# Kernel optimization log

Hardware: AMD Instinct MI355X
Metric: run time of the kernel (lower is better)

The kernel has to match this reference:

```python
import jax, jax.numpy as jnp
import numpy as np

K = 51           # kernel_size
DENSE_INNER = 2
EPS_LN = 1e-6
EPS_GRN = 1e-6

def _make_peripheral_coords(radius, dense_inner=2):
    coords = list(range(0, min(radius, dense_inner) + 1))
    v = 1
    while v < radius:
        v *= 2
        if v > dense_inner and v < radius:
            coords.append(v)
    if radius not in coords:
        coords.append(radius)
    return sorted(set(coords))

def _quantise(a, coords):
    q = 0
    for c in coords:
        if c <= a:
            q = c
        else:
            break
    return q

def _build_idx_map(kernel_size, dense_inner):
    radius = kernel_size // 2
    coords = _make_peripheral_coords(radius, dense_inner)
    signed = [-c for c in reversed(coords[1:])] + list(coords)
    P = len(signed)
    c2i = {c: i for i, c in enumerate(signed)}
    idx = []
    for i in range(kernel_size):
        oi = i - radius
        qi = _quantise(abs(oi), coords)
        ii = c2i[-qi if oi < 0 else qi]
        for j in range(kernel_size):
            oj = j - radius
            qj = _quantise(abs(oj), coords)
            jj = c2i[-qj if oj < 0 else qj]
            idx.append(ii * P + jj)
    return np.asarray(idx, dtype=np.int32), P

IDX_MAP, P = _build_idx_map(K, DENSE_INNER)  # P == 13 for K=51

DIM = 384
HID = 4 * DIM

def setup_inputs() -> dict:
    key = jax.random.key(0)
    ks = jax.random.split(key, 10)
    B, C, H, W = 8, DIM, 64, 64
    std = 0.02
    return {
        "x": jax.random.normal(ks[0], (B, C, H, W), jnp.float32),
        "weight_comp": jax.random.normal(ks[1], (C, P * P), jnp.float32) * std,
        "kpe": jax.random.normal(ks[2], (1, 1, K, K), jnp.float32) * std,
        "ln_w": jnp.ones((C,), jnp.float32),
        "ln_b": jnp.zeros((C,), jnp.float32),
        "w1": jax.random.normal(ks[3], (C, HID), jnp.float32) * std,
        "b1": jnp.zeros((HID,), jnp.float32),
        "grn_gamma": jax.random.normal(ks[4], (HID,), jnp.float32) * std,
        "grn_beta": jax.random.normal(ks[5], (HID,), jnp.float32) * std,
        "w2": jax.random.normal(ks[6], (HID, C), jnp.float32) * std,
        "b2": jnp.zeros((C,), jnp.float32),
    }

def _block(x, weight_comp, kpe, ln_w, ln_b, w1, b1, grn_gamma, grn_beta, w2, b2):
    C = x.shape[1]
    # gather-built peripheral depthwise kernel: (C, 1, K, K) + shared positional bias
    w = weight_comp[:, IDX_MAP].reshape(C, 1, K, K) + kpe
    y = jax.lax.conv_general_dilated(
        x, w, window_strides=(1, 1), padding=[(K // 2, K // 2)] * 2,
        feature_group_count=C, dimension_numbers=("NCHW", "OIHW", "NCHW"))
    h = y.transpose(0, 2, 3, 1)  # NHWC
    # LayerNorm (channels_last, biased variance, eps=1e-6)
    mu = jnp.mean(h, axis=-1, keepdims=True)
    var = jnp.mean(jnp.square(h - mu), axis=-1, keepdims=True)
    h = (h - mu) * jax.lax.rsqrt(var + EPS_LN) * ln_w + ln_b
    # pointwise MLP with GRN
    h = jnp.einsum("nhwc,cf->nhwf", h, w1) + b1
    h = jax.nn.gelu(h, approximate=False)  # nn.GELU default is exact erf form
    gx = jnp.sqrt(jnp.sum(jnp.square(h), axis=(1, 2), keepdims=True))  # (N,1,1,F)
    nx = gx / (jnp.mean(gx, axis=-1, keepdims=True) + EPS_GRN)
    h = grn_gamma * (h * nx) + grn_beta + h
    h = jnp.einsum("nhwf,fc->nhwc", h, w2) + b2
    return x + h.transpose(0, 3, 1, 2)

def reference(x, weight_comp, kpe, ln_w, ln_b, w1, b1, grn_gamma, grn_beta, w2, b2):
    return _block(x, weight_comp, kpe, ln_w, ln_b, w1, b1, grn_gamma, grn_beta, w2, b2)
```

## Files before the change

### kernel.cpp

```cpp
#include <hip/hip_runtime.h>

#define CDIM 384
#define FDIM 1536
#define KK 51
#define RAD 25
#define NPIX 32768
#define HW 4096

#define CSTR 136
#define OSTR 68

typedef float  f32x4  __attribute__((ext_vector_type(4)));
typedef short  short8 __attribute__((ext_vector_type(8)));
typedef __bf16 bf16x8 __attribute__((ext_vector_type(8)));
typedef unsigned short us4 __attribute__((ext_vector_type(4)));

__device__ __constant__ int AXIS[51] = {
  0,
  1,1,1,1,1,1,1,1,1,
  2,2,2,2,2,2,2,2,
  3,3,3,3,
  4,4,
  5,
  6,
  7,
  8,8,
  9,9,9,9,
  10,10,10,10,10,10,10,10,
  11,11,11,11,11,11,11,11,11,
  12
};

__device__ __forceinline__ unsigned short bf16_rn(float x){
  union { float f; unsigned u; } v; v.f = x;
  unsigned r = v.u + 0x7FFFu + ((v.u >> 16) & 1u);
  return (unsigned short)(r >> 16);
}
__device__ __forceinline__ unsigned short f2bf(float x){
  __bf16 h = (__bf16)x;
  return __builtin_bit_cast(unsigned short, h);
}
__device__ __forceinline__ float bf2f(unsigned short h){
  union { unsigned u; float f; } v; v.u = ((unsigned)h) << 16; return v.f;
}

__global__ __launch_bounds__(256) void k_prep(const float* __restrict__ wc,
                                              const float* __restrict__ kpe,
                                              float* __restrict__ wfull,
                                              const float* __restrict__ w1,
                                              unsigned short* __restrict__ w1T,
                                              const float* __restrict__ w2,
                                              unsigned short* __restrict__ w2T,
                                              const float* __restrict__ beta,
                                              const float* __restrict__ b2,
                                              float* __restrict__ c2,
                                              float* __restrict__ grn){
  __shared__ float tile[64][65];
  __shared__ float red[256];
  int bid = blockIdx.x;
  int tid = threadIdx.x;
  if (bid < 384){
    int c = bid;
    const float* wcc = wc + c*169;
    float* wo = wfull + (size_t)c*2601;
    for (int idx = tid; idx < 2601; idx += 256){
      int i = idx / 51, j = idx - i*51;
      wo[idx] = wcc[AXIS[i]*13 + AXIS[j]] + kpe[idx];
    }
  } else if (bid < 1056 - 384){
    const float* src; unsigned short* dst; int R, C, t;
    if (bid < 528){ src = w1; dst = w1T; R = CDIM; C = FDIM; t = bid - 384; }
    else          { src = w2; dst = w2T; R = FDIM; C = CDIM; t = bid - 528; }
    int nct = C >> 6;
    int tc = t % nct, tr = t / nct;
    int r0 = tr*64, c0 = tc*64;
    int lane = tid & 63, q = tid >> 6;
    #pragma unroll
    for (int it = 0; it < 16; ++it){
      int r = it*4 + q;
      tile[r][lane] = src[(size_t)(r0 + r)*C + c0 + lane];
    }
    __syncthreads();
    #pragma unroll
    for (int it = 0; it < 16; ++it){
      int c = it*4 + q;
      dst[(size_t)(c0 + c)*R + r0 + lane] = f2bf(tile[lane][c]);
    }
  } else if (bid < 1056){
    int c = bid - 672;
    float s = 0.f;
    for (int f = tid; f < FDIM; f += 256) s += beta[f] * w2[(size_t)f*CDIM + c];
    red[tid] = s;
    __syncthreads();
    for (int t = 128; t > 0; t >>= 1){
      if (tid < t) red[tid] += red[tid + t];
      __syncthreads();
    }
    if (tid == 0) c2[c] = red[0] + b2[c];
  } else {
    for (int i = tid; i < 8*FDIM; i += 256) grn[i] = 0.f;
  }
}

__global__ __launch_bounds__(256) void k_conv_mfma(const float* __restrict__ x,
                                                   const float* __restrict__ wfull,
                                                   float* __restrict__ y){
  __shared__ __align__(16) float outb[64*OSTR];
  __shared__ __align__(16) unsigned short bufs[2][4][1088];
  int img = blockIdx.x;
  int ch  = img % CDIM;
  const float* xim = x + (size_t)img*HW;
  const float* wch = wfull + (size_t)ch*2601;
  int tid = threadIdx.x;
  int lane = tid & 63, wid = tid >> 6;
  int li = lane & 15, g = lane >> 4;
  int t0 = (lane & 31) << 2;
  int c0 = lane >> 5;

  for (int i = tid; i < 1088; i += 256)
    *(f32x4*)&outb[i*4] = (f32x4){0.f,0.f,0.f,0.f};

  bf16x8 Bf[4][2];
  #pragma unroll
  for (int nt = 0; nt < 4; ++nt){
    int i = nt*16 + li;
    #pragma unroll
    for (int kt = 0; kt < 2; ++kt){
      union { bf16x8 v; unsigned short u[8]; } tmp;
      #pragma unroll
      for (int e = 0; e < 8; ++e){
        int j = kt*32 + g*8 + e;
        float v = (i < 51 && j < 51) ? wch[i*51 + j] : 0.f;
        tmp.u[e] = bf16_rn(v);
      }
      Bf[nt][kt] = tmp.v;
    }
  }

  {
    const float* xr = xim + (16*wid)*64;
    #pragma unroll
    for (int it = 0; it < 4; ++it){
      int c = c0 + 2*it;
      us4 o;
      #pragma unroll
      for (int e = 0; e < 4; ++e){
        int xi = t0 + e + c - 25;
        float v = (xi >= 0 && xi < 64) ? xr[xi] : 0.f;
        o[e] = bf16_rn(v);
      }
      *(us4*)&bufs[0][wid][c*CSTR + t0] = o;
    }
  }
  __syncthreads();

  #pragma unroll 1
  for (int ph = 0; ph < 16; ++ph){
    float pf[16];
    if (ph + 1 < 16){
      const float* xr = xim + (ph + 1 + 16*wid)*64;
      #pragma unroll
      for (int it = 0; it < 4; ++it){
        int c = c0 + 2*it;
        #pragma unroll
        for (int e = 0; e < 4; ++e){
          int xi = t0 + e + c - 25;
          int xc = min(max(xi, 0), 63);
          pf[it*4 + e] = xr[xc];
        }
      }
    }

    bf16x8 Af[4][2];
    #pragma unroll
    for (int s = 0; s < 4; ++s){
      const unsigned short* bb = &bufs[ph & 1][s][0];
      #pragma unroll
      for (int kt = 0; kt < 2; ++kt){
        int u0 = wid*16 + kt*32 + g*8 + li;
        int c  = li & 7;
        Af[s][kt] = *(const bf16x8*)&bb[c*CSTR + (u0 - c)];
      }
    }

    #pragma unroll
    for (int dd = 0; dd < 6; ++dd){
      int d = dd - 2;
      int pmax = ph + 25 + 16*d;
      if (pmax < 0 || pmax > 78) continue;
      f32x4 V = {0.f,0.f,0.f,0.f};
      #pragma unroll
      for (int s = 0; s < 4; ++s){
        int nt = s - d;
        if (nt < 0 || nt > 3) continue;
        V = __builtin_amdgcn_mfma_f32_16x16x32_bf16(Af[s][0], Bf[nt][0], V, 0, 0, 0);
        V = __builtin_amdgcn_mfma_f32_16x16x32_bf16(Af[s][1], Bf[nt][1], V, 0, 0, 0);
      }
      int p = pmax - li;
      if (p >= 0 && p < 64){
        float* oa = &outb[p*OSTR + wid*16 + g*4];
        f32x4 old = *(const f32x4*)oa;
        *(f32x4*)oa = old + V;
      }
    }

    if (ph + 1 < 16){
      unsigned short* dst = &bufs[(ph + 1) & 1][wid][0];
      #pragma unroll
      for (int it = 0; it < 4; ++it){
        int c = c0 + 2*it;
        us4 o;
        #pragma unroll
        for (int e = 0; e < 4; ++e){
          int xi = t0 + e + c - 25;
          float v = (xi >= 0 && xi < 64) ? pf[it*4 + e] : 0.f;
          o[e] = bf16_rn(v);
        }
        *(us4*)&dst[c*CSTR + t0] = o;
      }
    }
    __syncthreads();
  }

  float* yo = y + (size_t)img*HW;
  #pragma unroll
  for (int k = 0; k < 4; ++k){
    int pix = k*1024 + tid*4;
    int p = pix >> 6, q = pix & 63;
    *(f32x4*)(yo + pix) = *(const f32x4*)&outb[p*OSTR + q];
  }
}

__global__ __launch_bounds__(256) void k_ln(const float* __restrict__ y,
                                            const float* __restrict__ lnw,
                                            const float* __restrict__ lnb,
                                            unsigned short* __restrict__ yn){
  __shared__ float sred[2][4][64];
  __shared__ unsigned short tile[384*66];
  int tid = threadIdx.x, lane = tid & 63, w = tid >> 6;
  int pg0 = blockIdx.x * 64;
  int b = pg0 >> 12, sp0 = pg0 & 4095;
  const float* yb = y + (size_t)b*CDIM*HW + sp0 + lane;
  int cbase = w * 96;
  float sum = 0.f, sq = 0.f;
  for (int cc = 0; cc < 96; ++cc){
    float v = yb[(size_t)(cbase + cc)*HW];
    sum += v; sq += v*v;
  }
  sred[0][w][lane] = sum; sred[1][w][lane] = sq;
  __syncthreads();
  float ts = 0.f, tq = 0.f;
  #pragma unroll
  for (int u = 0; u < 4; ++u){ ts += sred[0][u][lane]; tq += sred[1][u][lane]; }
  float mu   = ts * (1.f/CDIM);
  float var  = tq * (1.f/CDIM) - mu*mu;
  float rstd = rsqrtf(var + 1e-6f);
  for (int cc = 0; cc < 96; ++cc){
    int c = cbase + cc;
    float v = (yb[(size_t)c*HW] - mu) * rstd * lnw[c] + lnb[c];
    tile[c*66 + lane] = f2bf(v);
  }
  __syncthreads();
  for (int pp = 0; pp < 16; ++pp){
    int p = w*16 + pp;
    size_t orow = (size_t)(pg0 + p)*CDIM;
    #pragma unroll
    for (int chk = 0; chk < 6; ++chk){
      yn[orow + chk*64 + lane] = tile[(chk*64 + lane)*66 + p];
    }
  }
}

__global__ __launch_bounds__(256) void k_gemm1p(const unsigned short* __restrict__ A,
                                                const unsigned short* __restrict__ BT,
                                                const float* __restrict__ b1,
                                                unsigned short* __restrict__ H,
                                                float* __restrict__ grn){
  __shared__ __align__(16) unsigned short pan[64*392];
  __shared__ __align__(16) unsigned short bS[2][128*40];
  int m0 = blockIdx.x * 64;
  int img = m0 >> 12;
  int tid = threadIdx.x;
  int lane = tid & 63, wid = tid >> 6;
  int wr = wid >> 1, wc = wid & 1;
  int lm = lane & 15, g = lane >> 4;
  int sr = tid & 127, sc = tid >> 7;

  #pragma unroll
  for (int t = 0; t < 12; ++t){
    int idx = tid + 256*t;
    int row = idx / 48, ch = idx - row*48;
    *(short8*)&pan[row*392 + ch*8] = *(const short8*)(A + (size_t)(m0 + row)*CDIM + ch*8);
  }

  {
    const unsigned short* gb = BT + (size_t)sr*CDIM + sc*16;
    *(short8*)&bS[0][sr*40 + sc*16]     = *(const short8*)(gb);
    *(short8*)&bS[0][sr*40 + sc*16 + 8] = *(const short8*)(gb + 8);
  }
  short8 rn0, rn1;
  {
    const unsigned short* gb = BT + (size_t)sr*CDIM + 32 + sc*16;
    rn0 = *(const short8*)(gb);
    rn1 = *(const short8*)(gb + 8);
  }
  int pft = 0, pk = 64;
  int par = 0;

  #pragma unroll 1
  for (int ft = 0; ft < 12; ++ft){
    f32x4 acc[2][4];
    #pragma unroll
    for (int i = 0; i < 2; ++i)
      #pragma unroll
      for (int j = 0; j < 4; ++j) acc[i][j] = (f32x4){0.f,0.f,0.f,0.f};

    #pragma unroll 1
    for (int ks = 0; ks < 12; ++ks){
      int k0 = ks*32;
      __syncthreads();
      if (!(ft == 11 && ks == 11)){
        *(short8*)&bS[par^1][sr*40 + sc*16]     = rn0;
        *(short8*)&bS[par^1][sr*40 + sc*16 + 8] = rn1;
      }
      if (!(ft == 11 && ks >= 10)){
        const unsigned short* gb = BT + (size_t)(pft*128 + sr)*CDIM + pk + sc*16;
        rn0 = *(const short8*)(gb);
        rn1 = *(const short8*)(gb + 8);
        pk += 32; if (pk == CDIM){ pk = 0; ++pft; }
      }
      bf16x8 aF[2], bF[4];
      #pragma unroll
      for (int fm = 0; fm < 2; ++fm) aF[fm] = *(const bf16x8*)&pan[(wr*32 + fm*16 + lm)*392 + k0 + g*8];
      #pragma unroll
      for (int fn = 0; fn < 4; ++fn) bF[fn] = *(const bf16x8*)&bS[par][(wc*64 + fn*16 + lm)*40 + g*8];
      #pragma unroll
      for (int fm = 0; fm < 2; ++fm)
        #pragma unroll
        for (int fn = 0; fn < 4; ++fn)
          acc[fm][fn] = __builtin_amdgcn_mfma_f32_16x16x32_bf16(aF[fm], bF[fn], acc[fm][fn], 0, 0, 0);
      par ^= 1;
    }

    int n0 = ft*128;
    float psum[4] = {0.f,0.f,0.f,0.f};
    #pragma unroll
    for (int fn = 0; fn < 4; ++fn){
      int n = n0 + wc*64 + fn*16 + lm;
      float bias = b1[n];
      #pragma unroll
      for (int fm = 0; fm < 2; ++fm){
        int mb = m0 + wr*32 + fm*16 + g*4;
        #pragma unroll
        for (int r = 0; r < 4; ++r){
          float v = acc[fm][fn][r] + bias;
          v = 0.5f * v * (1.f + erff(v * 0.70710678118654752f));
          H[(size_t)(mb + r)*FDIM + n] = f2bf(v);
          psum[fn] += v*v;
        }
      }
    }
    #pragma unroll
    for (int fn = 0; fn < 4; ++fn){
      float v = psum[fn];
      v += __shfl_xor(v, 16);
      v += __shfl_xor(v, 32);
      if (g == 0){
        atomicAdd(&grn[img*FDIM + n0 + wc*64 + fn*16 + lm], v);
      }
    }
  }
}

__global__ __launch_bounds__(256) void k_grn(const float* __restrict__ grn,
                                             const float* __restrict__ gamma,
                                             float* __restrict__ S){
  int n = blockIdx.x;
  const float* g = grn + n*FDIM;
  __shared__ float red[256];
  float p = 0.f;
  for (int f = threadIdx.x; f < FDIM; f += 256) p += sqrtf(g[f]);
  red[threadIdx.x] = p;
  __syncthreads();
  for (int s = 128; s > 0; s >>= 1){
    if (threadIdx.x < s) red[threadIdx.x] += red[threadIdx.x + s];
    __syncthreads();
  }
  float mean = red[0] * (1.f/FDIM);
  float inv = 1.f/(mean + 1e-6f);
  for (int f = threadIdx.x; f < FDIM; f += 256){
    float nx = sqrtf(g[f]) * inv;
    S[n*FDIM + f] = 1.f + gamma[f]*nx;
  }
}

__global__ __launch_bounds__(256) void k_gemm2(const unsigned short* __restrict__ W2T,
                                               const unsigned short* __restrict__ H,
                                               const float* __restrict__ S,
                                               const float* __restrict__ c2,
                                               const float* __restrict__ xg,
                                               float* __restrict__ out){
  __shared__ __align__(16) unsigned short aS[2][128*40];
  __shared__ __align__(16) unsigned short bS[2][128*40];
  int bid = blockIdx.x;
  int bm = bid % 3;
  int bn = bid / 3;
  int c0 = bm*128, p0 = bn*128;
  int img = p0 >> 12;
  const float* Simg = S + img*FDIM;
  int tid = threadIdx.x;
  int lane = tid & 63, wid = tid >> 6;
  int wr = wid >> 1, wc = wid & 1;
  int lm = lane & 15, g = lane >> 4;
  int sr = tid & 127, sc = tid >> 7;
  f32x4 acc[4][4];
  #pragma unroll
  for (int i = 0; i < 4; ++i)
    #pragma unroll
    for (int j = 0; j < 4; ++j) acc[i][j] = (f32x4){0.f,0.f,0.f,0.f};

  {
    const unsigned short* ga = W2T + (size_t)(c0 + sr)*FDIM + sc*16;
    *(short8*)&aS[0][sr*40 + sc*16]     = *(const short8*)(ga);
    *(short8*)&aS[0][sr*40 + sc*16 + 8] = *(const short8*)(ga + 8);
    const unsigned short* gb = H + (size_t)(p0 + sr)*FDIM + sc*16;
    short8 h0 = *(const short8*)(gb);
    short8 h1 = *(const short8*)(gb + 8);
    const float* sv = Simg + sc*16;
    short8 o0, o1;
    #pragma unroll
    for (int e = 0; e < 8; ++e){
      o0[e] = (short)f2bf(bf2f((unsigned short)h0[e]) * sv[e]);
      o1[e] = (short)f2bf(bf2f((unsigned short)h1[e]) * sv[e+8]);
    }
    *(short8*)&bS[0][sr*40 + sc*16]     = o0;
    *(short8*)&bS[0][sr*40 + sc*16 + 8] = o1;
  }
  short8 ra0, ra1, rh0, rh1;
  f32x4 rs0, rs1, rs2, rs3;
  {
    const unsigned short* ga = W2T + (size_t)(c0 + sr)*FDIM + 32 + sc*16;
    ra0 = *(const short8*)(ga); ra1 = *(const short8*)(ga + 8);
    const unsigned short* gb = H + (size_t)(p0 + sr)*FDIM + 32 + sc*16;
    rh0 = *(const short8*)(gb); rh1 = *(const short8*)(gb + 8);
    const float* sv = Simg + 32 + sc*16;
    rs0 = *(const f32x4*)(sv);      rs1 = *(const f32x4*)(sv + 4);
    rs2 = *(const f32x4*)(sv + 8);  rs3 = *(const f32x4*)(sv + 12);
  }
  int par = 0;

  #pragma unroll 1
  for (int ks = 0; ks < 48; ++ks){
    __syncthreads();
    if (ks + 1 < 48){
      *(short8*)&aS[par^1][sr*40 + sc*16]     = ra0;
      *(short8*)&aS[par^1][sr*40 + sc*16 + 8] = ra1;
      short8 o0, o1;
      float se[16];
      #pragma unroll
      for (int e = 0; e < 4; ++e){ se[e]=rs0[e]; se[4+e]=rs1[e]; se[8+e]=rs2[e]; se[12+e]=rs3[e]; }
      #pragma unroll
      for (int e = 0; e < 8; ++e){
        o0[e] = (short)f2bf(bf2f((unsigned short)rh0[e]) * se[e]);
        o1[e] = (short)f2bf(bf2f((unsigned short)rh1[e]) * se[e+8]);
      }
      *(short8*)&bS[par^1][sr*40 + sc*16]     = o0;
      *(short8*)&bS[par^1][sr*40 + sc*16 + 8] = o1;
    }
    if (ks + 2 < 48){
      int nk = (ks + 2)*32;
      const unsigned short* ga = W2T + (size_t)(c0 + sr)*FDIM + nk + sc*16;
      ra0 = *(const short8*)(ga); ra1 = *(const short8*)(ga + 8);
      const unsigned short* gb = H + (size_t)(p0 + sr)*FDIM + nk + sc*16;
      rh0 = *(const short8*)(gb); rh1 = *(const short8*)(gb + 8);
      const float* sv = Simg + nk + sc*16;
      rs0 = *(const f32x4*)(sv);      rs1 = *(const f32x4*)(sv + 4);
      rs2 = *(const f32x4*)(sv + 8);  rs3 = *(const f32x4*)(sv + 12);
    }
    bf16x8 aF[4], bF[4];
    #pragma unroll
    for (int fm = 0; fm < 4; ++fm) aF[fm] = *(const bf16x8*)&aS[par][(wr*64 + fm*16 + lm)*40 + g*8];
    #pragma unroll
    for (int fn = 0; fn < 4; ++fn) bF[fn] = *(const bf16x8*)&bS[par][(wc*64 + fn*16 + lm)*40 + g*8];
    #pragma unroll
    for (int fm = 0; fm < 4; ++fm)
      #pragma unroll
      for (int fn = 0; fn < 4; ++fn)
        acc[fm][fn] = __builtin_amdgcn_mfma_f32_16x16x32_bf16(aF[fm], bF[fn], acc[fm][fn], 0, 0, 0);
    par ^= 1;
  }

  int sp0 = p0 & 4095;
  #pragma unroll
  for (int fn = 0; fn < 4; ++fn){
    int pixoff = sp0 + wc*64 + fn*16 + lm;
    #pragma unroll
    for (int fm = 0; fm < 4; ++fm){
      #pragma unroll
      for (int r = 0; r < 4; ++r){
        int c = c0 + wr*64 + fm*16 + g*4 + r;
        size_t addr = ((size_t)img*CDIM + c)*HW + pixoff;
        out[addr] = acc[fm][fn][r] + c2[c] + xg[addr];
      }
    }
  }
}

extern "C" void kernel_launch(void* const* d_in, const int* in_sizes, int n_in,
                              void* d_out, int out_size, void* d_ws, size_t ws_size,
                              hipStream_t stream) {
  const float* x    = (const float*)d_in[0];
  const float* wc   = (const float*)d_in[1];
  const float* kpe  = (const float*)d_in[2];
  const float* lnw  = (const float*)d_in[3];
  const float* lnb  = (const float*)d_in[4];
  const float* w1   = (const float*)d_in[5];
  const float* b1   = (const float*)d_in[6];
  const float* gam  = (const float*)d_in[7];
  const float* beta = (const float*)d_in[8];
  const float* w2   = (const float*)d_in[9];
  const float* b2   = (const float*)d_in[10];
  float* out = (float*)d_out;

  char* ws = (char*)d_ws;
  size_t o = 0;
  auto take = [&](size_t bytes)->char*{
    char* p = ws + o;
    o = (o + bytes + 511) & ~(size_t)511;
    return p;
  };
  float*          y     = out;
  float*          wfull = (float*)take((size_t)CDIM*2601*4);
  unsigned short* yn    = (unsigned short*)take((size_t)NPIX*CDIM*2);
  unsigned short* H     = (unsigned short*)take((size_t)NPIX*FDIM*2);
  unsigned short* w1T   = (unsigned short*)take((size_t)CDIM*FDIM*2);
  unsigned short* w2T   = (unsigned short*)take((size_t)CDIM*FDIM*2);
  float*          grn   = (float*)take(8*FDIM*4);
  float*          S     = (float*)take(8*FDIM*4);
  float*          c2    = (float*)take(CDIM*4);
  if (o > ws_size) return;

  k_prep<<<1057, 256, 0, stream>>>(wc, kpe, wfull, w1, w1T, w2, w2T, beta, b2, c2, grn);
  k_conv_mfma<<<3072, 256, 0, stream>>>(x, wfull, y);
  k_ln<<<NPIX/64, 256, 0, stream>>>(y, lnw, lnb, yn);
  k_gemm1p<<<NPIX/64, 256, 0, stream>>>(yn, w1T, b1, H, grn);
  k_grn<<<8, 256, 0, stream>>>(grn, gam, S);
  k_gemm2<<<3*(NPIX/128), 256, 0, stream>>>(w2T, H, S, c2, x, out);
}
```

Measured before the change: 401.1 us.

## Use tanh-form GELU, restructure bias reduction blocks, remap gemm2 block order

Swaps the exact erf GELU in the first GEMM epilogue for the tanh approximation, computed with a fast exponential as a sigmoid. The c2 = beta·w2 + b2 reduction moves from one block per channel to 64 channels per block, cutting k_prep from 1057 to 679 blocks. The k_gemm2 block index is remapped so that 8 consecutive blocks cover different pixel tiles, which changes cache locality across XCDs. The tanh GELU only approximates the exact form the reference asks for, adding a small numerical error.

```diff
diff --git a/kernel.cpp b/kernel.cpp
--- a/kernel.cpp
+++ b/kernel.cpp
@@ -42,6 +42,11 @@
 }
 __device__ __forceinline__ float bf2f(unsigned short h){
   union { unsigned u; float f; } v; v.u = ((unsigned)h) << 16; return v.f;
+}
+__device__ __forceinline__ float gelu_f(float v){
+  float t = v*(0.7978845608f + 0.0356774081f*v*v);
+  float sg = 1.f/(1.f + __expf(-2.f*t));
+  return v * sg;
 }
 
 __global__ __launch_bounds__(256) void k_prep(const float* __restrict__ wc,
@@ -67,7 +72,7 @@
       int i = idx / 51, j = idx - i*51;
       wo[idx] = wcc[AXIS[i]*13 + AXIS[j]] + kpe[idx];
     }
-  } else if (bid < 1056 - 384){
+  } else if (bid < 672){
     const float* src; unsigned short* dst; int R, C, t;
     if (bid < 528){ src = w1; dst = w1T; R = CDIM; C = FDIM; t = bid - 384; }
     else          { src = w2; dst = w2T; R = FDIM; C = CDIM; t = bid - 528; }
@@ -86,17 +91,18 @@
       int c = it*4 + q;
       dst[(size_t)(c0 + c)*R + r0 + lane] = f2bf(tile[lane][c]);
     }
-  } else if (bid < 1056){
-    int c = bid - 672;
+  } else if (bid < 678){
+    int lane = tid & 63, w = tid >> 6;
+    int c = (bid - 672)*64 + lane;
     float s = 0.f;
-    for (int f = tid; f < FDIM; f += 256) s += beta[f] * w2[(size_t)f*CDIM + c];
-    red[tid] = s;
+    for (int f = w*384; f < (w + 1)*384; ++f)
+      s += beta[f] * w2[(size_t)f*CDIM + c];
+    red[w*64 + lane] = s;
     __syncthreads();
-    for (int t = 128; t > 0; t >>= 1){
-      if (tid < t) red[tid] += red[tid + t];
-      __syncthreads();
-    }
-    if (tid == 0) c2[c] = red[0] + b2[c];
+    if (tid < 64){
+      float t = red[tid] + red[64 + tid] + red[128 + tid] + red[192 + tid];
+      c2[c] = t + b2[c];
+    }
   } else {
     for (int i = tid; i < 8*FDIM; i += 256) grn[i] = 0.f;
   }
@@ -353,8 +359,7 @@
         int mb = m0 + wr*32 + fm*16 + g*4;
         #pragma unroll
         for (int r = 0; r < 4; ++r){
-          float v = acc[fm][fn][r] + bias;
-          v = 0.5f * v * (1.f + erff(v * 0.70710678118654752f));
+          float v = gelu_f(acc[fm][fn][r] + bias);
           H[(size_t)(mb + r)*FDIM + n] = f2bf(v);
           psum[fn] += v*v;
         }
@@ -403,8 +408,10 @@
   __shared__ __align__(16) unsigned short aS[2][128*40];
   __shared__ __align__(16) unsigned short bS[2][128*40];
   int bid = blockIdx.x;
-  int bm = bid % 3;
-  int bn = bid / 3;
+  int x8 = bid & 7;
+  int kk = bid >> 3;
+  int bm = kk % 3;
+  int bn = x8 + 8*(kk / 3);
   int c0 = bm*128, p0 = bn*128;
   int img = p0 >> 12;
   const float* Simg = S + img*FDIM;
@@ -540,7 +547,7 @@
   float*          c2    = (float*)take(CDIM*4);
   if (o > ws_size) return;
 
-  k_prep<<<1057, 256, 0, stream>>>(wc, kpe, wfull, w1, w1T, w2, w2T, beta, b2, c2, grn);
+  k_prep<<<679, 256, 0, stream>>>(wc, kpe, wfull, w1, w1T, w2, w2T, beta, b2, c2, grn);
   k_conv_mfma<<<3072, 256, 0, stream>>>(x, wfull, y);
   k_ln<<<NPIX/64, 256, 0, stream>>>(y, lnw, lnb, yn);
   k_gemm1p<<<NPIX/64, 256, 0, stream>>>(yn, w1T, b1, H, grn);
```

New measurement: 402.0 us. No clear change (+0.2%).
